# Kernel optimization log

Hardware: AMD Instinct MI355X
Metric: run time of the kernel (lower is better)

The kernel has to match this reference:

```python
import jax, jax.numpy as jnp
import numpy as np

THRE = 4.0  # ReLUX threshold / multispike lens
EPS = 1e-5  # BatchNorm eps (torch default)

@jax.custom_vjp
def spike(x):
    # multispike forward: floor(clamp(x,0,4)+0.5)
    return jnp.floor(jnp.clip(x, 0.0, THRE) + 0.5)

def _spike_fwd(x):
    return spike(x), x

def _spike_bwd(x, g):
    # surrogate gradient: pass-through on 0 < x < lens
    return (g * ((x > 0) & (x < THRE)).astype(g.dtype),)

spike.defvjp(_spike_fwd, _spike_bwd)


def setup_inputs() -> dict:
    key = jax.random.key(0)
    k0, k1, k2 = jax.random.split(key, 3)
    B, N, C = 4, 1024, 512
    x = jax.random.normal(k0, (B, N, C), jnp.float32)
    Wqkv = jax.random.normal(k1, (3 * C, C), jnp.float32) * (C ** -0.5)  # Linear weight [out,in], no bias
    gamma = jnp.ones((3 * C,), jnp.float32)   # BN weight
    beta = jnp.zeros((3 * C,), jnp.float32)   # BN bias
    Wproj = jax.random.normal(k2, (C, C), jnp.float32) * (C ** -0.5)
    bproj = jnp.zeros((C,), jnp.float32)
    return {"x": x, "Wqkv": Wqkv, "gamma": gamma, "beta": beta, "Wproj": Wproj, "bproj": bproj}


def reference(x, Wqkv, gamma, beta, Wproj, bproj):
    B, N, C = x.shape
    H = 8
    hd = C // H
    scale = hd ** -0.5

    xs = spike(x)                                    # head_spike
    qkv = jnp.einsum('bnc,dc->bnd', xs, Wqkv)        # [B,N,3C]
    # BatchNorm1d over channel dim with batch stats across (B, N)
    mu = qkv.mean(axis=(0, 1))
    var = qkv.var(axis=(0, 1))
    qkv = (qkv - mu) * jax.lax.rsqrt(var + EPS) * gamma + beta

    qkv = qkv.reshape(B, N, 3, H, hd).transpose(2, 0, 3, 1, 4)  # [3,B,H,N,hd]
    q = spike(qkv[0])
    k = spike(qkv[1])
    v = spike(qkv[2])

    attn = jnp.einsum('bhnd,bhmd->bhnm', q, k)       # no softmax
    attn = spike(attn)
    out = jnp.einsum('bhnm,bhmd->bhnd', attn, v) * scale
    out = out.transpose(0, 2, 1, 3).reshape(B, N, C)
    out = spike(out)                                 # project_spike
    return jnp.einsum('bnc,dc->bnd', out, Wproj) + bproj
```

## Files before the change

kernel.cpp:

```cpp
#include <hip/hip_runtime.h>

typedef __attribute__((ext_vector_type(8))) short short8;
typedef __attribute__((ext_vector_type(4))) short short4v;
typedef __attribute__((ext_vector_type(4))) float f32x4;
typedef __attribute__((ext_vector_type(4))) int int4v;
typedef __attribute__((ext_vector_type(4))) unsigned int u32x4;

#define THRE 4.0f

#define GLOAD_LDS16(g, l) \
    __builtin_amdgcn_global_load_lds((const __attribute__((address_space(1))) void*)(g), \
                                     (__attribute__((address_space(3))) void*)(l), 16, 0, 0)

__device__ __forceinline__ float spikef(float x) {
    return floorf(fminf(fmaxf(x, 0.0f), THRE) + 0.5f);
}
__device__ __forceinline__ unsigned short f2bf(float f) {
    return (unsigned short)(__builtin_bit_cast(unsigned int, f) >> 16);
}
__device__ __forceinline__ unsigned short f2bf_rn(float f) {
    unsigned u = __builtin_bit_cast(unsigned int, f);
    unsigned r = ((u >> 16) & 1u) + 0x7FFFu;
    return (unsigned short)((u + r) >> 16);
}
__device__ __forceinline__ float bf2f(unsigned short s) {
    return __builtin_bit_cast(float, (unsigned int)s << 16);
}
__device__ __forceinline__ int4v mfma_i8(u32x4 a, u32x4 b, int4v c) {
    return __builtin_amdgcn_mfma_i32_16x16x64_i8(__builtin_bit_cast(int4v, a),
                                                 __builtin_bit_cast(int4v, b), c, 0, 0, 0);
}

__global__ void k_prep(const float* __restrict__ x,
                       const float* __restrict__ Wq, const float* __restrict__ Wp,
                       short* __restrict__ xs, short* __restrict__ Wqd, short* __restrict__ Wpd) {
    int i = blockIdx.x * 256 + threadIdx.x;
    if (i < 524288) {
        const float4 v = *(const float4*)&x[(size_t)i * 4];
        short4v o;
        o.x = (short)f2bf(spikef(v.x));
        o.y = (short)f2bf(spikef(v.y));
        o.z = (short)f2bf(spikef(v.z));
        o.w = (short)f2bf(spikef(v.w));
        *(short4v*)&xs[(size_t)i * 4] = o;
    } else if (i < 720896) {
        const size_t j = (size_t)(i - 524288) * 4;
        const float4 v = *(const float4*)&Wq[j];
        short4v o;
        o.x = (short)(__builtin_bit_cast(unsigned int, v.x) >> 16);
        o.y = (short)(__builtin_bit_cast(unsigned int, v.y) >> 16);
        o.z = (short)(__builtin_bit_cast(unsigned int, v.z) >> 16);
        o.w = (short)(__builtin_bit_cast(unsigned int, v.w) >> 16);
        *(short4v*)&Wqd[j] = o;
    } else {
        const size_t j = (size_t)(i - 720896) * 4;
        const float4 v = *(const float4*)&Wp[j];
        short4v o;
        o.x = (short)(__builtin_bit_cast(unsigned int, v.x) >> 16);
        o.y = (short)(__builtin_bit_cast(unsigned int, v.y) >> 16);
        o.z = (short)(__builtin_bit_cast(unsigned int, v.z) >> 16);
        o.w = (short)(__builtin_bit_cast(unsigned int, v.w) >> 16);
        *(short4v*)&Wpd[j] = o;
    }
}

__global__ __launch_bounds__(256) void k_gemm_qkv(const short* __restrict__ A,
                                                  const short* __restrict__ B,
                                                  short* __restrict__ C,
                                                  float* __restrict__ psum,
                                                  float* __restrict__ psq) {
    __shared__ __align__(16) short As[128 * 64];
    __shared__ __align__(16) short Bs[96 * 64];
    const int tid  = threadIdx.x;
    const int lane = tid & 63, wv = tid >> 6;
    const int wy = wv >> 1, wx = wv & 1;
    const int quad = lane >> 4, l16 = lane & 15;
    const int u = blockIdx.x;
    const int mtile = u & 31;
    const int m0 = mtile * 128, n0 = (u >> 5) * 96;
    const int K = 512, N = 1536;

    f32x4 acc[4][3];
    #pragma unroll
    for (int i = 0; i < 4; ++i)
        #pragma unroll
        for (int j = 0; j < 3; ++j)
            #pragma unroll
            for (int r = 0; r < 4; ++r) acc[i][j][r] = 0.f;

    const short* gA[4]; short* lA[4];
    #pragma unroll
    for (int i = 0; i < 4; ++i) {
        int L = wv + 4 * i;
        int c = L * 64 + lane;
        int r = c >> 3, g = (c & 7) ^ (r & 7);
        gA[i] = A + (size_t)(m0 + r) * K + g * 8;
        lA[i] = &As[L * 512];
    }
    const short* gB[3]; short* lB[3];
    #pragma unroll
    for (int i = 0; i < 3; ++i) {
        int L = wv + 4 * i;
        int c = L * 64 + lane;
        int r = c >> 3, g = (c & 7) ^ (r & 7);
        gB[i] = B + (size_t)(n0 + r) * K + g * 8;
        lB[i] = &Bs[L * 512];
    }

    for (int k0 = 0; k0 < K; k0 += 64) {
        __syncthreads();
        #pragma unroll
        for (int i = 0; i < 4; ++i) GLOAD_LDS16(gA[i] + k0, lA[i]);
        #pragma unroll
        for (int i = 0; i < 3; ++i) GLOAD_LDS16(gB[i] + k0, lB[i]);
        __syncthreads();
        #pragma unroll
        for (int sub = 0; sub < 2; ++sub) {
            const int jc = (sub * 4 + quad) ^ (l16 & 7);
            short8 aF[4], bF[3];
            #pragma unroll
            for (int mt = 0; mt < 4; ++mt)
                aF[mt] = *(const short8*)&As[(wy * 64 + mt * 16 + l16) * 64 + jc * 8];
            #pragma unroll
            for (int nt = 0; nt < 3; ++nt)
                bF[nt] = *(const short8*)&Bs[(wx * 48 + nt * 16 + l16) * 64 + jc * 8];
            #pragma unroll
            for (int mt = 0; mt < 4; ++mt)
                #pragma unroll
                for (int nt = 0; nt < 3; ++nt)
                    acc[mt][nt] = __builtin_amdgcn_mfma_f32_16x16x32_bf16(aF[mt], bF[nt], acc[mt][nt], 0, 0, 0);
        }
    }

    #pragma unroll
    for (int mt = 0; mt < 4; ++mt)
        #pragma unroll
        for (int r = 0; r < 4; ++r) {
            int row = m0 + wy * 64 + mt * 16 + quad * 4 + r;
            short* Cr = C + (size_t)row * N + n0 + wx * 48 + l16;
            #pragma unroll
            for (int nt = 0; nt < 3; ++nt) Cr[nt * 16] = (short)f2bf_rn(acc[mt][nt][r]);
        }

    __syncthreads();
    float* PS = (float*)As;
    float* PQ = (float*)Bs;
    #pragma unroll
    for (int nt = 0; nt < 3; ++nt) {
        float s = 0.f, q = 0.f;
        #pragma unroll
        for (int mt = 0; mt < 4; ++mt)
            #pragma unroll
            for (int r = 0; r < 4; ++r) {
                float v = acc[mt][nt][r];
                s += v;
                q = fmaf(v, v, q);
            }
        PS[(wy * 4 + quad) * 96 + wx * 48 + nt * 16 + l16] = s;
        PQ[(wy * 4 + quad) * 96 + wx * 48 + nt * 16 + l16] = q;
    }
    __syncthreads();
    if (tid < 96) {
        float s = 0.f, q = 0.f;
        #pragma unroll
        for (int i = 0; i < 8; ++i) { s += PS[i * 96 + tid]; q += PQ[i * 96 + tid]; }
        psum[mtile * 1536 + n0 + tid] = s;
        psq [mtile * 1536 + n0 + tid] = q;
    }
}

template<bool BIAS, int MT, int NT>
__global__ __launch_bounds__(256) void k_gemm_bf16(const short* __restrict__ A,
                                                   const short* __restrict__ B,
                                                   const float* __restrict__ bias,
                                                   float* __restrict__ C,
                                                   int M, int N, int K) {
    constexpr int BM = MT * 32, BN = NT * 32;
    __shared__ __align__(16) short As[BM * 32];
    __shared__ __align__(16) short Bs[BN * 32];
    const int tid  = threadIdx.x;
    const int lane = tid & 63, wv = tid >> 6;
    const int wy = wv >> 1, wx = wv & 1;
    const int quad = lane >> 4, l16 = lane & 15;
    const int m0 = blockIdx.y * BM, n0 = blockIdx.x * BN;

    f32x4 acc[MT][NT];
    #pragma unroll
    for (int i = 0; i < MT; ++i)
        #pragma unroll
        for (int j = 0; j < NT; ++j)
            #pragma unroll
            for (int r = 0; r < 4; ++r) acc[i][j][r] = 0.f;

    constexpr int LA = 2 * MT, LB = 2 * NT;
    const short* gA[(LA + 3) / 4]; short* lA[(LA + 3) / 4]; int nA = 0;
    #pragma unroll
    for (int L0 = 0; L0 < LA; L0 += 4) {
        int L = L0 + wv;
        if (L < LA) {
            int c = L * 64 + lane;
            gA[nA] = A + (size_t)(m0 + (c >> 2)) * K + (c & 3) * 8;
            lA[nA] = &As[L * 512];
            ++nA;
        }
    }
    const short* gB[(LB + 3) / 4]; short* lB[(LB + 3) / 4]; int nB = 0;
    #pragma unroll
    for (int L0 = 0; L0 < LB; L0 += 4) {
        int L = L0 + wv;
        if (L < LB) {
            int c = L * 64 + lane;
            gB[nB] = B + (size_t)(n0 + (c >> 2)) * K + (c & 3) * 8;
            lB[nB] = &Bs[L * 512];
            ++nB;
        }
    }

    for (int k0 = 0; k0 < K; k0 += 32) {
        __syncthreads();
        for (int i = 0; i < nA; ++i) GLOAD_LDS16(gA[i] + k0, lA[i]);
        for (int i = 0; i < nB; ++i) GLOAD_LDS16(gB[i] + k0, lB[i]);
        __syncthreads();
        short8 aF[MT], bF[NT];
        #pragma unroll
        for (int mt = 0; mt < MT; ++mt)
            aF[mt] = *(const short8*)&As[(wy * MT * 16 + mt * 16 + l16) * 32 + quad * 8];
        #pragma unroll
        for (int nt = 0; nt < NT; ++nt)
            bF[nt] = *(const short8*)&Bs[(wx * NT * 16 + nt * 16 + l16) * 32 + quad * 8];
        #pragma unroll
        for (int mt = 0; mt < MT; ++mt)
            #pragma unroll
            for (int nt = 0; nt < NT; ++nt)
                acc[mt][nt] = __builtin_amdgcn_mfma_f32_16x16x32_bf16(aF[mt], bF[nt], acc[mt][nt], 0, 0, 0);
    }

    float bs[NT];
    #pragma unroll
    for (int nt = 0; nt < NT; ++nt) bs[nt] = BIAS ? bias[n0 + wx * NT * 16 + nt * 16 + l16] : 0.f;
    #pragma unroll
    for (int mt = 0; mt < MT; ++mt)
        #pragma unroll
        for (int r = 0; r < 4; ++r) {
            int row = m0 + wy * MT * 16 + mt * 16 + quad * 4 + r;
            float* Cr = C + (size_t)row * N + n0 + wx * NT * 16 + l16;
            #pragma unroll
            for (int nt = 0; nt < NT; ++nt) Cr[nt * 16] = acc[mt][nt][r] + bs[nt];
        }
}

__global__ __launch_bounds__(256) void k_bn_spike(const short* __restrict__ qkvb,
                           const float* __restrict__ psum, const float* __restrict__ psq,
                           const float* __restrict__ gamma, const float* __restrict__ beta,
                           unsigned char* __restrict__ qp, unsigned char* __restrict__ kp,
                           unsigned char* __restrict__ vt) {
    __shared__ float sa[64], sb[64];
    __shared__ __align__(16) unsigned char tile[64 * 80];
    const int tid = threadIdx.x;
    const int slice = blockIdx.x;
    const int c0 = slice * 64;
    const int r0 = blockIdx.y * 256;
    const int b = r0 >> 10, nb = r0 & 1023;

    if (tid < 64) {
        const int c = c0 + tid;
        double s = 0.0, q = 0.0;
        for (int st = 0; st < 32; ++st) { s += (double)psum[st * 1536 + c]; q += (double)psq[st * 1536 + c]; }
        const double mu  = s / 4096.0;
        const double var = q / 4096.0 - mu * mu;
        const float a = (float)((double)gamma[c] / sqrt(var + 1e-5));
        sa[tid] = a;
        sb[tid] = fmaf(-(float)mu, a, beta[c]);
    }
    __syncthreads();

    const int ch = tid & 63, rq = tid >> 6;
    const float A = sa[ch], Bsh = sb[ch];

    if (slice < 16) {
        const int h = slice & 7;
        unsigned char* base = (slice < 8 ? qp : kp) + (((size_t)b * 8 + h) * 1024 + nb) * 64;
        for (int i = rq; i < 256; i += 4) {
            float v = bf2f((unsigned short)qkvb[(size_t)(r0 + i) * 1536 + c0 + ch]);
            base[(size_t)i * 64 + ch] = (unsigned char)spikef(fmaf(v, A, Bsh));
        }
    } else {
        const int h = slice - 16;
        const int e = tid >> 2, j0 = (tid & 3) * 16;
        unsigned char* vbase = vt + (((size_t)b * 8 + h) * 64 + e) * 1024 + nb;
        for (int rb = 0; rb < 4; ++rb) {
            __syncthreads();
            for (int i = rq; i < 64; i += 4) {
                float v = bf2f((unsigned short)qkvb[(size_t)(r0 + rb * 64 + i) * 1536 + c0 + ch]);
                tile[ch * 80 + i] = (unsigned char)spikef(fmaf(v, A, Bsh));
            }
            __syncthreads();
            *(u32x4*)&vbase[rb * 64 + j0] = *(const u32x4*)&tile[e * 80 + j0];
        }
    }
}

__global__ __launch_bounds__(256) void k_attn(const unsigned char* __restrict__ qp,
                                              const unsigned char* __restrict__ kp,
                                              const unsigned char* __restrict__ vt,
                                              short* __restrict__ sout) {
    __shared__ __align__(16) unsigned char SM[54272];
    unsigned char* Qs = SM;
    unsigned char* Ks = SM + 4096;
    unsigned char* Vs = SM + 20480;
    unsigned int* Sb = (unsigned int*)(SM + 36864);
    const int tid  = threadIdx.x;
    const int lane = tid & 63, w = tid >> 6;
    const int quad = lane >> 4, l16 = lane & 15;
    const int u = blockIdx.x;
    const int bhid = u & 31;
    const int b = bhid >> 3, h = bhid & 7;
    const int n0 = (u >> 5) * 64;
    const size_t bh = (size_t)b * 8 + h;

    {
        const int r = tid >> 2, p = tid & 3;
        const int g = p ^ (r & 3) ^ ((r >> 2) & 3);
        GLOAD_LDS16(qp + (bh * 1024 + n0 + r) * 64 + g * 16, Qs + (size_t)tid * 16);
    }
    const unsigned char* gK[4]; unsigned char* lK[4];
    const unsigned char* gV[4]; unsigned char* lV[4];
    #pragma unroll
    for (int i = 0; i < 4; ++i) {
        int c = tid + 256 * i;
        int rk = c >> 2, pk2 = c & 3;
        int gk = pk2 ^ (rk & 3) ^ ((rk >> 2) & 3);
        gK[i] = kp + (bh * 1024 + rk) * 64 + gk * 16;
        lK[i] = Ks + (size_t)c * 16;
        int rv = c >> 4, pv = c & 15;
        int gv = pv ^ (rv & 15);
        gV[i] = vt + (bh * 64 + rv) * 1024 + gv * 16;
        lV[i] = Vs + (size_t)c * 16;
    }
    __syncthreads();
    u32x4 qf[4];
    {
        const int pq = quad ^ (l16 & 3) ^ ((l16 >> 2) & 3);
        #pragma unroll
        for (int mt = 0; mt < 4; ++mt)
            qf[mt] = *(const u32x4*)&Qs[(mt * 16 + l16) * 64 + pq * 16];
    }

    int4v of[4];
    #pragma unroll
    for (int mt = 0; mt < 4; ++mt)
        #pragma unroll
        for (int r = 0; r < 4; ++r) of[mt][r] = 0;

    const int pk = quad ^ (l16 & 3) ^ ((l16 >> 2) & 3);

    for (int j0 = 0; j0 < 1024; j0 += 256) {
        __syncthreads();
        #pragma unroll
        for (int i = 0; i < 4; ++i) {
            GLOAD_LDS16(gK[i] + (size_t)j0 * 64, lK[i]);
            GLOAD_LDS16(gV[i] + j0, lV[i]);
        }
        __syncthreads();

        #pragma unroll
        for (int jt = 0; jt < 4; ++jt) {
            u32x4 kf = *(const u32x4*)&Ks[(w * 64 + jt * 16 + l16) * 64 + pk * 16];
            #pragma unroll
            for (int mt = 0; mt < 4; ++mt) {
                int4v z;
                #pragma unroll
                for (int r = 0; r < 4; ++r) z[r] = 0;
                int4v s = mfma_i8(kf, qf[mt], z);
                unsigned int pkk = 0;
                #pragma unroll
                for (int r = 0; r < 4; ++r) {
                    int v = s[r]; v = v < 0 ? 0 : (v > 4 ? 4 : v);
                    pkk |= (unsigned int)v << (8 * r);
                }
                Sb[(mt * 16 + l16) * 68 + w * 16 + jt * 4 + quad] = pkk;
            }
        }
        __syncthreads();

        #pragma unroll
        for (int kk = 0; kk < 4; ++kk) {
            const int pv = (kk * 4 + quad) ^ l16;
            u32x4 bV = *(const u32x4*)&Vs[(w * 16 + l16) * 256 + pv * 16];
            #pragma unroll
            for (int mt = 0; mt < 4; ++mt) {
                u32x4 aS = *(const u32x4*)&Sb[(mt * 16 + l16) * 68 + kk * 16 + quad * 4];
                of[mt] = mfma_i8(aS, bV, of[mt]);
            }
        }
    }

    #pragma unroll
    for (int mt = 0; mt < 4; ++mt)
        #pragma unroll
        for (int r = 0; r < 4; ++r) {
            size_t orow = (size_t)b * 1024 + n0 + mt * 16 + quad * 4 + r;
            sout[orow * 512 + h * 64 + w * 16 + l16] =
                (short)f2bf(spikef((float)of[mt][r] * 0.125f));
        }
}

extern "C" void kernel_launch(void* const* d_in, const int* in_sizes, int n_in,
                              void* d_out, int out_size, void* d_ws, size_t ws_size,
                              hipStream_t stream) {
    const float* x     = (const float*)d_in[0];
    const float* Wqkv  = (const float*)d_in[1];
    const float* gamma = (const float*)d_in[2];
    const float* beta  = (const float*)d_in[3];
    const float* Wproj = (const float*)d_in[4];
    const float* bproj = (const float*)d_in[5];
    float* out = (float*)d_out;

    char* w = (char*)d_ws;
    short* xs            = (short*)(w);
    short* Wqkv2         = (short*)(w + 8388608);
    short* Wproj2        = (short*)(w + 11534336);
    short* qkvb          = (short*)(w + 12582912);
    unsigned char* qp    = (unsigned char*)(w + 37748736);
    unsigned char* kp    = (unsigned char*)(w + 41943040);
    unsigned char* vt    = (unsigned char*)(w + 46137344);
    float* psum          = (float*)(w + 50331648);
    float* psq           = psum + 32 * 1536;
    short* sout          = xs;

    k_prep<<<3072, 256, 0, stream>>>(x, Wqkv, Wproj, xs, Wqkv2, Wproj2);
    k_gemm_qkv<<<512, 256, 0, stream>>>(xs, Wqkv2, qkvb, psum, psq);
    k_bn_spike<<<dim3(24, 16), 256, 0, stream>>>(qkvb, psum, psq, gamma, beta, qp, kp, vt);
    k_attn<<<512, 256, 0, stream>>>(qp, kp, vt, sout);
    k_gemm_bf16<true, 1, 4><<<dim3(4, 128), 256, 0, stream>>>(
        sout, Wproj2, bproj, out, 4096, 512, 512);
}
```

Before: 116.1 us.

## Quantize QKV GEMM to int8 with per-row weight scales

Spiked inputs are stored as uint8 (values 0-4) and Wqkv is quantized to int8 with a per-output-row absmax scale. The QKV GEMM then runs on the i8 MFMA 16x16x64 with a 128-wide K tile, and the epilogue dequantizes with the row scale before writing bf16 and the BN partial sums. This halves operand bytes and doubles MFMA throughput per instruction. The cost is weight quantization error, which is coarser than the earlier bf16 truncation and can flip spike thresholds downstream.

```diff
diff --git a/kernel.cpp b/kernel.cpp
--- a/kernel.cpp
+++ b/kernel.cpp
@@ -2,6 +2,8 @@
 
 typedef __attribute__((ext_vector_type(8))) short short8;
 typedef __attribute__((ext_vector_type(4))) short short4v;
+typedef __attribute__((ext_vector_type(8))) signed char s8x8;
+typedef __attribute__((ext_vector_type(4))) unsigned char u8x4;
 typedef __attribute__((ext_vector_type(4))) float f32x4;
 typedef __attribute__((ext_vector_type(4))) int int4v;
 typedef __attribute__((ext_vector_type(4))) unsigned int u32x4;
@@ -33,44 +35,54 @@
 
 __global__ void k_prep(const float* __restrict__ x,
                        const float* __restrict__ Wq, const float* __restrict__ Wp,
-                       short* __restrict__ xs, short* __restrict__ Wqd, short* __restrict__ Wpd) {
-    int i = blockIdx.x * 256 + threadIdx.x;
-    if (i < 524288) {
+                       unsigned char* __restrict__ xs8, signed char* __restrict__ Wq8,
+                       float* __restrict__ wscale, short* __restrict__ Wpd) {
+    const int blk = blockIdx.x, tid = threadIdx.x;
+    if (blk < 2048) {
+        const int i = blk * 256 + tid;
         const float4 v = *(const float4*)&x[(size_t)i * 4];
-        short4v o;
-        o.x = (short)f2bf(spikef(v.x));
-        o.y = (short)f2bf(spikef(v.y));
-        o.z = (short)f2bf(spikef(v.z));
-        o.w = (short)f2bf(spikef(v.w));
-        *(short4v*)&xs[(size_t)i * 4] = o;
-    } else if (i < 720896) {
-        const size_t j = (size_t)(i - 524288) * 4;
-        const float4 v = *(const float4*)&Wq[j];
+        u8x4 o;
+        o.x = (unsigned char)spikef(v.x);
+        o.y = (unsigned char)spikef(v.y);
+        o.z = (unsigned char)spikef(v.z);
+        o.w = (unsigned char)spikef(v.w);
+        *(u8x4*)&xs8[(size_t)i * 4] = o;
+    } else if (blk < 2432) {
+        const int row = (blk - 2048) * 4 + (tid >> 6);
+        const int lane = tid & 63;
+        const float* wr = Wq + (size_t)row * 512 + lane * 8;
+        float w[8];
+        float mx = 0.f;
+        #pragma unroll
+        for (int i = 0; i < 8; ++i) { w[i] = wr[i]; mx = fmaxf(mx, fabsf(w[i])); }
+        #pragma unroll
+        for (int o = 32; o > 0; o >>= 1) mx = fmaxf(mx, __shfl_xor(mx, o, 64));
+        const float inv = mx > 0.f ? 127.0f / mx : 0.f;
+        s8x8 q;
+        #pragma unroll
+        for (int i = 0; i < 8; ++i) q[i] = (signed char)rintf(w[i] * inv);
+        *(s8x8*)&Wq8[(size_t)row * 512 + lane * 8] = q;
+        if (lane == 0) wscale[row] = mx > 0.f ? mx / 127.0f : 0.f;
+    } else {
+        const int i = (blk - 2432) * 256 + tid;
+        const float4 v = *(const float4*)&Wp[(size_t)i * 4];
         short4v o;
         o.x = (short)(__builtin_bit_cast(unsigned int, v.x) >> 16);
         o.y = (short)(__builtin_bit_cast(unsigned int, v.y) >> 16);
         o.z = (short)(__builtin_bit_cast(unsigned int, v.z) >> 16);
         o.w = (short)(__builtin_bit_cast(unsigned int, v.w) >> 16);
-        *(short4v*)&Wqd[j] = o;
-    } else {
-        const size_t j = (size_t)(i - 720896) * 4;
-        const float4 v = *(const float4*)&Wp[j];
-        short4v o;
-        o.x = (short)(__builtin_bit_cast(unsigned int, v.x) >> 16);
-        o.y = (short)(__builtin_bit_cast(unsigned int, v.y) >> 16);
-        o.z = (short)(__builtin_bit_cast(unsigned int, v.z) >> 16);
-        o.w = (short)(__builtin_bit_cast(unsigned int, v.w) >> 16);
-        *(short4v*)&Wpd[j] = o;
-    }
-}
-
-__global__ __launch_bounds__(256) void k_gemm_qkv(const short* __restrict__ A,
-                                                  const short* __restrict__ B,
+        *(short4v*)&Wpd[(size_t)i * 4] = o;
+    }
+}
+
+__global__ __launch_bounds__(256) void k_gemm_qkv(const unsigned char* __restrict__ A,
+                                                  const signed char* __restrict__ B,
+                                                  const float* __restrict__ wscale,
                                                   short* __restrict__ C,
                                                   float* __restrict__ psum,
                                                   float* __restrict__ psq) {
-    __shared__ __align__(16) short As[128 * 64];
-    __shared__ __align__(16) short Bs[96 * 64];
+    __shared__ __align__(16) unsigned char As[128 * 128];
+    __shared__ __align__(16) unsigned char Bs[96 * 128];
     const int tid  = threadIdx.x;
     const int lane = tid & 63, wv = tid >> 6;
     const int wy = wv >> 1, wx = wv & 1;
@@ -78,36 +90,36 @@
     const int u = blockIdx.x;
     const int mtile = u & 31;
     const int m0 = mtile * 128, n0 = (u >> 5) * 96;
-    const int K = 512, N = 1536;
-
-    f32x4 acc[4][3];
+    const int N = 1536;
+
+    int4v acc[4][3];
     #pragma unroll
     for (int i = 0; i < 4; ++i)
         #pragma unroll
         for (int j = 0; j < 3; ++j)
             #pragma unroll
-            for (int r = 0; r < 4; ++r) acc[i][j][r] = 0.f;
-
-    const short* gA[4]; short* lA[4];
+            for (int r = 0; r < 4; ++r) acc[i][j][r] = 0;
+
+    const unsigned char* gA[4]; unsigned char* lA[4];
     #pragma unroll
     for (int i = 0; i < 4; ++i) {
         int L = wv + 4 * i;
         int c = L * 64 + lane;
         int r = c >> 3, g = (c & 7) ^ (r & 7);
-        gA[i] = A + (size_t)(m0 + r) * K + g * 8;
-        lA[i] = &As[L * 512];
-    }
-    const short* gB[3]; short* lB[3];
+        gA[i] = A + (size_t)(m0 + r) * 512 + g * 16;
+        lA[i] = &As[(size_t)c * 16];
+    }
+    const unsigned char* gB[3]; unsigned char* lB[3];
     #pragma unroll
     for (int i = 0; i < 3; ++i) {
         int L = wv + 4 * i;
         int c = L * 64 + lane;
         int r = c >> 3, g = (c & 7) ^ (r & 7);
-        gB[i] = B + (size_t)(n0 + r) * K + g * 8;
-        lB[i] = &Bs[L * 512];
-    }
-
-    for (int k0 = 0; k0 < K; k0 += 64) {
+        gB[i] = (const unsigned char*)B + (size_t)(n0 + r) * 512 + g * 16;
+        lB[i] = &Bs[(size_t)c * 16];
+    }
+
+    for (int k0 = 0; k0 < 512; k0 += 128) {
         __syncthreads();
         #pragma unroll
         for (int i = 0; i < 4; ++i) GLOAD_LDS16(gA[i] + k0, lA[i]);
@@ -115,23 +127,31 @@
         for (int i = 0; i < 3; ++i) GLOAD_LDS16(gB[i] + k0, lB[i]);
         __syncthreads();
         #pragma unroll
-        for (int sub = 0; sub < 2; ++sub) {
-            const int jc = (sub * 4 + quad) ^ (l16 & 7);
-            short8 aF[4], bF[3];
-            #pragma unroll
-            for (int mt = 0; mt < 4; ++mt)
-                aF[mt] = *(const short8*)&As[(wy * 64 + mt * 16 + l16) * 64 + jc * 8];
-            #pragma unroll
-            for (int nt = 0; nt < 3; ++nt)
-                bF[nt] = *(const short8*)&Bs[(wx * 48 + nt * 16 + l16) * 64 + jc * 8];
+        for (int kk = 0; kk < 2; ++kk) {
+            u32x4 aF[4], bF[3];
+            #pragma unroll
+            for (int mt = 0; mt < 4; ++mt) {
+                const int r = wy * 64 + mt * 16 + l16;
+                aF[mt] = *(const u32x4*)&As[(size_t)r * 128 + (((kk * 4 + quad) ^ (r & 7)) * 16)];
+            }
+            #pragma unroll
+            for (int nt = 0; nt < 3; ++nt) {
+                const int r = wx * 48 + nt * 16 + l16;
+                bF[nt] = *(const u32x4*)&Bs[(size_t)r * 128 + (((kk * 4 + quad) ^ (r & 7)) * 16)];
+            }
             #pragma unroll
             for (int mt = 0; mt < 4; ++mt)
                 #pragma unroll
                 for (int nt = 0; nt < 3; ++nt)
-                    acc[mt][nt] = __builtin_amdgcn_mfma_f32_16x16x32_bf16(aF[mt], bF[nt], acc[mt][nt], 0, 0, 0);
-        }
-    }
-
+                    acc[mt][nt] = mfma_i8(aF[mt], bF[nt], acc[mt][nt]);
+        }
+    }
+
+    float sc[3];
+    #pragma unroll
+    for (int nt = 0; nt < 3; ++nt) sc[nt] = wscale[n0 + wx * 48 + nt * 16 + l16];
+
+    float vacc[4][3][4];
     #pragma unroll
     for (int mt = 0; mt < 4; ++mt)
         #pragma unroll
@@ -139,7 +159,11 @@
             int row = m0 + wy * 64 + mt * 16 + quad * 4 + r;
             short* Cr = C + (size_t)row * N + n0 + wx * 48 + l16;
             #pragma unroll
-            for (int nt = 0; nt < 3; ++nt) Cr[nt * 16] = (short)f2bf_rn(acc[mt][nt][r]);
+            for (int nt = 0; nt < 3; ++nt) {
+                float v = (float)acc[mt][nt][r] * sc[nt];
+                vacc[mt][nt][r] = v;
+                Cr[nt * 16] = (short)f2bf_rn(v);
+            }
         }
 
     __syncthreads();
@@ -152,7 +176,7 @@
         for (int mt = 0; mt < 4; ++mt)
             #pragma unroll
             for (int r = 0; r < 4; ++r) {
-                float v = acc[mt][nt][r];
+                float v = vacc[mt][nt][r];
                 s += v;
                 q = fmaf(v, v, q);
             }
@@ -417,8 +441,9 @@
     float* out = (float*)d_out;
 
     char* w = (char*)d_ws;
-    short* xs            = (short*)(w);
-    short* Wqkv2         = (short*)(w + 8388608);
+    unsigned char* xs8   = (unsigned char*)(w);
+    signed char* Wq8     = (signed char*)(w + 8388608);
+    float* wscale        = (float*)(w + 9437184);
     short* Wproj2        = (short*)(w + 11534336);
     short* qkvb          = (short*)(w + 12582912);
     unsigned char* qp    = (unsigned char*)(w + 37748736);
@@ -426,10 +451,10 @@
     unsigned char* vt    = (unsigned char*)(w + 46137344);
     float* psum          = (float*)(w + 50331648);
     float* psq           = psum + 32 * 1536;
-    short* sout          = xs;
-
-    k_prep<<<3072, 256, 0, stream>>>(x, Wqkv, Wproj, xs, Wqkv2, Wproj2);
-    k_gemm_qkv<<<512, 256, 0, stream>>>(xs, Wqkv2, qkvb, psum, psq);
+    short* sout          = (short*)(w);
+
+    k_prep<<<2688, 256, 0, stream>>>(x, Wqkv, Wproj, xs8, Wq8, wscale, Wproj2);
+    k_gemm_qkv<<<512, 256, 0, stream>>>(xs8, Wq8, wscale, qkvb, psum, psq);
     k_bn_spike<<<dim3(24, 16), 256, 0, stream>>>(qkvb, psum, psq, gamma, beta, qp, kp, vt);
     k_attn<<<512, 256, 0, stream>>>(qp, kp, vt, sout);
     k_gemm_bf16<true, 1, 4><<<dim3(4, 128), 256, 0, stream>>>(
```

Measured after the change: 113.3 us. 1.02x faster.
